# Kernel tuning notes

Hardware: AMD Instinct MI355X
Metric: run time of the kernel (lower is better)

The kernel has to match this reference:

```python
import jax, jax.numpy as jnp
import numpy as np

NEG_SLOPE = 0.01  # torch nn.LeakyReLU default


def setup_inputs() -> dict:
    key = jax.random.key(0)
    k1, k2, k3 = jax.random.split(key, 3)
    B, H, D, L = 4, 8, 64, 2048
    q = jax.random.normal(k1, (B, H, D, L), dtype=jnp.float32)
    k = jax.random.normal(k2, (B, H, D, L), dtype=jnp.float32)
    v = jax.random.normal(k3, (B, H, D, L), dtype=jnp.float32)
    return {"q": q, "k": k, "v": v}


def reference(q, k, v):
    # q, k, v: [B, H, D, L] (note: feature dim BEFORE length, as in the torch module)
    d_tensor = q.shape[2]
    scale = 1.0 / np.sqrt(d_tensor).astype(np.float32)
    # scores = LeakyReLU(q^T k / sqrt(d)) : [B, H, Lq, Lk]
    scores = jnp.einsum('bhdq,bhdk->bhqk', q, k) * scale
    scores = jax.nn.leaky_relu(scores, negative_slope=NEG_SLOPE)
    psi = jax.nn.softmax(scores, axis=-1)
    # out = (psi @ v^T)^T : [B, H, D, Lq]
    out = jnp.einsum('bhqk,bhdk->bhdq', psi, v)
    return out
```

## Files before the change

kernel.cpp:

```cpp
#include <hip/hip_runtime.h>
#include <math.h>

#define DD 64
#define LL 2048
#define TQ 128
#define TK 64
#define NTHREADS 512
#define QSCALE 0.18033688011112042f

typedef __bf16 bf16_t;
typedef __bf16 bf16x8 __attribute__((ext_vector_type(8)));
typedef float f32x16 __attribute__((ext_vector_type(16)));

struct __align__(16) SMemA {
  bf16_t Qs[TQ][72];
  bf16_t Ks[TK][72];
  bf16_t Vs[DD][72];
};
union __align__(16) SMemU {
  SMemA a;
  float Oe[TQ][65];
};

__global__ __launch_bounds__(NTHREADS, 4)
void attn_flash_bf16(const float* __restrict__ q, const float* __restrict__ k,
                     const float* __restrict__ v, float* __restrict__ out) {
  __shared__ SMemU sm;
  __shared__ float rs1[TQ];
  const int tid  = threadIdx.x;
  const int w    = tid >> 6;
  const int lane = tid & 63;
  const int l31  = lane & 31;
  const int hh   = lane >> 5;
  const int strip = w & 3;
  const int half  = w >> 2;
  const int wbase = strip * 32;
  const int lkh   = half * 32;
  const int head = blockIdx.y;
  const int q0   = blockIdx.x * TQ;
  const size_t hoff = (size_t)head * DD * LL;
  const float* qp = q + hoff;
  const float* kp = k + hoff;
  const float* vp = v + hoff;

  {
    int lq  = tid & 127;
    int d0q = (tid >> 7) * 16;
    const float* src = qp + q0 + lq;
    for (int g = 0; g < 2; ++g) {
      bf16x8 pk;
      for (int j = 0; j < 8; ++j)
        pk[j] = (bf16_t)(src[(size_t)(d0q + g * 8 + j) * LL] * QSCALE);
      *(bf16x8*)&sm.a.Qs[lq][d0q + g * 8] = pk;
    }
  }

  const int klk = tid & 63;
  const int kd0 = (tid >> 6) * 8;
  const int vd  = tid >> 3;
  const int vc8 = (tid & 7) * 8;

  float  kreg[8];
  float4 vreg[2];
  {
    const float* ks = kp + klk;
    for (int j = 0; j < 8; ++j) kreg[j] = ks[(size_t)(kd0 + j) * LL];
    vreg[0] = *(const float4*)(vp + (size_t)vd * LL + vc8);
    vreg[1] = *(const float4*)(vp + (size_t)vd * LL + vc8 + 4);
  }

  __syncthreads();
  bf16x8 bq[4];
  for (int kk = 0; kk < 4; ++kk)
    bq[kk] = *(const bf16x8*)&sm.a.Qs[wbase + l31][kk * 16 + 8 * hh];

  f32x16 oacc[2];
  for (int dt = 0; dt < 2; ++dt)
    for (int r = 0; r < 16; ++r) oacc[dt][r] = 0.f;
  float rsum = 0.f;

  for (int t = 0; t < LL / TK; ++t) {
    __syncthreads();
    {
      bf16x8 pk;
      for (int j = 0; j < 8; ++j) pk[j] = (bf16_t)kreg[j];
      *(bf16x8*)&sm.a.Ks[klk][kd0] = pk;
      bf16x8 pv;
      pv[0] = (bf16_t)vreg[0].x; pv[1] = (bf16_t)vreg[0].y;
      pv[2] = (bf16_t)vreg[0].z; pv[3] = (bf16_t)vreg[0].w;
      pv[4] = (bf16_t)vreg[1].x; pv[5] = (bf16_t)vreg[1].y;
      pv[6] = (bf16_t)vreg[1].z; pv[7] = (bf16_t)vreg[1].w;
      *(bf16x8*)&sm.a.Vs[vd][vc8] = pv;
    }
    __syncthreads();

    if (t + 1 < LL / TK) {
      const int lk0n = (t + 1) * TK;
      const float* ks = kp + lk0n + klk;
      for (int j = 0; j < 8; ++j) kreg[j] = ks[(size_t)(kd0 + j) * LL];
      vreg[0] = *(const float4*)(vp + (size_t)vd * LL + lk0n + vc8);
      vreg[1] = *(const float4*)(vp + (size_t)vd * LL + lk0n + vc8 + 4);
    }

    f32x16 st;
    for (int r = 0; r < 16; ++r) st[r] = 0.f;
    for (int kk = 0; kk < 4; ++kk) {
      bf16x8 ak = *(const bf16x8*)&sm.a.Ks[lkh + l31][kk * 16 + 8 * hh];
      st = __builtin_amdgcn_mfma_f32_32x32x16_bf16(ak, bq[kk], st, 0, 0, 0);
    }

    unsigned pb[8];
    for (int r = 0; r < 16; ++r) {
      float s = st[r];
      s = fmaxf(s, 0.01f * s);
      float p = __builtin_amdgcn_exp2f(s);
      rsum += p;
      st[r] = p;
    }
    for (int qq = 0; qq < 8; ++qq) {
      union { bf16_t b[2]; unsigned u; } pk;
      pk.b[0] = (bf16_t)st[2 * qq];
      pk.b[1] = (bf16_t)st[2 * qq + 1];
      pb[qq] = pk.u;
    }

    for (int kk2 = 0; kk2 < 2; ++kk2) {
      unsigned l0 = pb[4 * kk2 + 0], l1 = pb[4 * kk2 + 1];
      unsigned l2 = pb[4 * kk2 + 2], l3 = pb[4 * kk2 + 3];
      unsigned s0 = hh ? l0 : l2;
      unsigned s1 = hh ? l1 : l3;
      unsigned f0 = (unsigned)__shfl_xor((int)s0, 32);
      unsigned f1 = (unsigned)__shfl_xor((int)s1, 32);
      union { unsigned u[4]; bf16x8 v; } ap;
      ap.u[0] = hh ? f0 : l0;
      ap.u[1] = hh ? f1 : l1;
      ap.u[2] = hh ? l2 : f0;
      ap.u[3] = hh ? l3 : f1;
      const int lkb = lkh + kk2 * 16 + 8 * hh;
      for (int dt = 0; dt < 2; ++dt) {
        bf16x8 bv = *(const bf16x8*)&sm.a.Vs[dt * 32 + l31][lkb];
        oacc[dt] = __builtin_amdgcn_mfma_f32_32x32x16_bf16(ap.v, bv, oacc[dt], 0, 0, 0);
      }
    }
  }

  float rtot = rsum + __shfl_xor(rsum, 32);
  __syncthreads();
  if (half == 1) {
    rs1[wbase + l31] = rtot;
    for (int r = 0; r < 16; ++r) {
      int row = (r & 3) + 8 * (r >> 2) + 4 * hh;
      for (int dt = 0; dt < 2; ++dt)
        sm.Oe[wbase + row][dt * 32 + l31] = oacc[dt][r];
    }
  }
  __syncthreads();
  if (half == 0) {
    float tot = rtot + rs1[wbase + l31];
    rs1[wbase + l31] = 1.0f / tot;
    float inv[16];
    for (int r = 0; r < 16; ++r) {
      int row = (r & 3) + 8 * (r >> 2) + 4 * hh;
      inv[r] = rs1[wbase + row];
    }
    for (int r = 0; r < 16; ++r) {
      int row = (r & 3) + 8 * (r >> 2) + 4 * hh;
      for (int dt = 0; dt < 2; ++dt) {
        int col = dt * 32 + l31;
        sm.Oe[wbase + row][col] = (oacc[dt][r] + sm.Oe[wbase + row][col]) * inv[r];
      }
    }
  }
  __syncthreads();
  float* op = out + hoff + q0;
  for (int i = 0; i < 16; ++i) {
    int idx = tid + NTHREADS * i;
    int d   = idx >> 7;
    int lq  = idx & 127;
    op[(size_t)d * LL + lq] = sm.Oe[lq][d];
  }
}

extern "C" void kernel_launch(void* const* d_in, const int* in_sizes, int n_in,
                              void* d_out, int out_size, void* d_ws, size_t ws_size,
                              hipStream_t stream) {
  const float* q = (const float*)d_in[0];
  const float* k = (const float*)d_in[1];
  const float* v = (const float*)d_in[2];
  float* out = (float*)d_out;
  dim3 grid(LL / TQ, 32);
  attn_flash_bf16<<<grid, NTHREADS, 0, stream>>>(q, k, v, out);
}
```

Baseline: 144.7 us.

## Pre-convert Q/K/V to transposed bf16 and double-buffer K/V tiles

Adds a prep kernel that converts Q and K to bf16 with a length-major transposed layout and V to bf16, writing them into workspace. The attention kernel then loads 16-byte contiguous bf16 vectors instead of strided fp32 scalars, uses double-buffered K/V shared tiles so one barrier per iteration is removed, and raises wave priority around MFMA blocks. This costs an extra kernel launch and a full read/write pass over the inputs. It also depends on workspace being available, otherwise the old kernel runs.

```diff
diff --git a/kernel.cpp b/kernel.cpp
--- a/kernel.cpp
+++ b/kernel.cpp
@@ -3,6 +3,7 @@
 
 #define DD 64
 #define LL 2048
+#define HEADS 32
 #define TQ 128
 #define TK 64
 #define NTHREADS 512
@@ -11,6 +12,202 @@
 typedef __bf16 bf16_t;
 typedef __bf16 bf16x8 __attribute__((ext_vector_type(8)));
 typedef float f32x16 __attribute__((ext_vector_type(16)));
+
+__global__ __launch_bounds__(256)
+void prep_bf16(const float* __restrict__ q, const float* __restrict__ k,
+               const float* __restrict__ v, bf16_t* __restrict__ qt,
+               bf16_t* __restrict__ kt, bf16_t* __restrict__ vb) {
+  __shared__ float ld[64][65];
+  const int t = threadIdx.x;
+  const int which = blockIdx.z;
+  const int head = blockIdx.y;
+  const int l0 = blockIdx.x * 64;
+  const size_t hoff = (size_t)head * DD * LL;
+  if (which == 2) {
+    const float* src = v + hoff;
+    bf16_t* dst = vb + hoff;
+    const int lp = (t & 31) * 2;
+    const int db = (t >> 5) * 8;
+    for (int i = 0; i < 8; ++i) {
+      int d = db + i;
+      float2 x = *(const float2*)(src + (size_t)d * LL + l0 + lp);
+      union { bf16_t b[2]; unsigned u; } pk;
+      pk.b[0] = (bf16_t)x.x;
+      pk.b[1] = (bf16_t)x.y;
+      *(unsigned*)(dst + (size_t)d * LL + l0 + lp) = pk.u;
+    }
+  } else {
+    const float* src = (which == 0) ? (q + hoff) : (k + hoff);
+    bf16_t* dst = (which == 0) ? (qt + hoff) : (kt + hoff);
+    const float scale = (which == 0) ? QSCALE : 1.0f;
+    const int l = t & 63;
+    const int db = (t >> 6) * 16;
+    for (int i = 0; i < 16; ++i) {
+      int d = db + i;
+      ld[l][d] = src[(size_t)d * LL + l0 + l] * scale;
+    }
+    __syncthreads();
+    const int dp = (t & 31) * 2;
+    const int lb = (t >> 5) * 8;
+    for (int i = 0; i < 8; ++i) {
+      int lw = lb + i;
+      union { bf16_t b[2]; unsigned u; } pk;
+      pk.b[0] = (bf16_t)ld[lw][dp];
+      pk.b[1] = (bf16_t)ld[lw][dp + 1];
+      *(unsigned*)(dst + (size_t)(l0 + lw) * DD + dp) = pk.u;
+    }
+  }
+}
+
+struct __align__(16) SMemA2 {
+  bf16_t Qs[TQ][72];
+  bf16_t Ks[2][TK][72];
+  bf16_t Vs[2][DD][72];
+};
+union __align__(16) SMemU2 {
+  SMemA2 a;
+  float Oe[TQ][65];
+};
+
+__global__ __launch_bounds__(NTHREADS, 4)
+void attn_flash_bf16_v2(const bf16_t* __restrict__ qt, const bf16_t* __restrict__ kt,
+                        const bf16_t* __restrict__ vb, float* __restrict__ out) {
+  __shared__ SMemU2 sm;
+  __shared__ float rs1[TQ];
+  const int tid  = threadIdx.x;
+  const int w    = tid >> 6;
+  const int lane = tid & 63;
+  const int l31  = lane & 31;
+  const int hh   = lane >> 5;
+  const int strip = w & 3;
+  const int half  = w >> 2;
+  const int wbase = strip * 32;
+  const int lkh   = half * 32;
+  const int head = blockIdx.y;
+  const int q0   = blockIdx.x * TQ;
+  const size_t hoff = (size_t)head * DD * LL;
+  const bf16_t* qp = qt + hoff;
+  const bf16_t* kp = kt + hoff;
+  const bf16_t* vp = vb + hoff;
+
+  for (int g = 0; g < 2; ++g) {
+    int c  = tid + NTHREADS * g;
+    int lq = c >> 3;
+    int d0 = (c & 7) * 8;
+    bf16x8 x = *(const bf16x8*)(qp + (size_t)(q0 + lq) * DD + d0);
+    *(bf16x8*)&sm.a.Qs[lq][d0] = x;
+  }
+
+  const int srow = tid >> 3;
+  const int scol = (tid & 7) * 8;
+
+  bf16x8 kreg = *(const bf16x8*)(kp + (size_t)srow * DD + scol);
+  bf16x8 vreg = *(const bf16x8*)(vp + (size_t)srow * LL + scol);
+
+  __syncthreads();
+  bf16x8 bq[4];
+  for (int kk = 0; kk < 4; ++kk)
+    bq[kk] = *(const bf16x8*)&sm.a.Qs[wbase + l31][kk * 16 + 8 * hh];
+
+  f32x16 oacc[2];
+  for (int dt = 0; dt < 2; ++dt)
+    for (int r = 0; r < 16; ++r) oacc[dt][r] = 0.f;
+  float rsum = 0.f;
+
+  for (int t = 0; t < LL / TK; ++t) {
+    const int cur = t & 1;
+    *(bf16x8*)&sm.a.Ks[cur][srow][scol] = kreg;
+    *(bf16x8*)&sm.a.Vs[cur][srow][scol] = vreg;
+    __syncthreads();
+
+    if (t + 1 < LL / TK) {
+      const int lk0n = (t + 1) * TK;
+      kreg = *(const bf16x8*)(kp + (size_t)(lk0n + srow) * DD + scol);
+      vreg = *(const bf16x8*)(vp + (size_t)srow * LL + lk0n + scol);
+    }
+
+    f32x16 st;
+    for (int r = 0; r < 16; ++r) st[r] = 0.f;
+    __builtin_amdgcn_s_setprio(1);
+    for (int kk = 0; kk < 4; ++kk) {
+      bf16x8 ak = *(const bf16x8*)&sm.a.Ks[cur][lkh + l31][kk * 16 + 8 * hh];
+      st = __builtin_amdgcn_mfma_f32_32x32x16_bf16(ak, bq[kk], st, 0, 0, 0);
+    }
+    __builtin_amdgcn_s_setprio(0);
+
+    unsigned pb[8];
+    for (int r = 0; r < 16; ++r) {
+      float s = st[r];
+      s = fmaxf(s, 0.01f * s);
+      float p = __builtin_amdgcn_exp2f(s);
+      rsum += p;
+      st[r] = p;
+    }
+    for (int qq = 0; qq < 8; ++qq) {
+      union { bf16_t b[2]; unsigned u; } pk;
+      pk.b[0] = (bf16_t)st[2 * qq];
+      pk.b[1] = (bf16_t)st[2 * qq + 1];
+      pb[qq] = pk.u;
+    }
+
+    for (int kk2 = 0; kk2 < 2; ++kk2) {
+      unsigned l0 = pb[4 * kk2 + 0], l1 = pb[4 * kk2 + 1];
+      unsigned l2 = pb[4 * kk2 + 2], l3 = pb[4 * kk2 + 3];
+      unsigned s0 = hh ? l0 : l2;
+      unsigned s1 = hh ? l1 : l3;
+      unsigned f0 = (unsigned)__shfl_xor((int)s0, 32);
+      unsigned f1 = (unsigned)__shfl_xor((int)s1, 32);
+      union { unsigned u[4]; bf16x8 v; } ap;
+      ap.u[0] = hh ? f0 : l0;
+      ap.u[1] = hh ? f1 : l1;
+      ap.u[2] = hh ? l2 : f0;
+      ap.u[3] = hh ? l3 : f1;
+      const int lkb = lkh + kk2 * 16 + 8 * hh;
+      __builtin_amdgcn_s_setprio(1);
+      for (int dt = 0; dt < 2; ++dt) {
+        bf16x8 bv = *(const bf16x8*)&sm.a.Vs[cur][dt * 32 + l31][lkb];
+        oacc[dt] = __builtin_amdgcn_mfma_f32_32x32x16_bf16(ap.v, bv, oacc[dt], 0, 0, 0);
+      }
+      __builtin_amdgcn_s_setprio(0);
+    }
+  }
+
+  float rtot = rsum + __shfl_xor(rsum, 32);
+  __syncthreads();
+  if (half == 1) {
+    rs1[wbase + l31] = rtot;
+    for (int r = 0; r < 16; ++r) {
+      int row = (r & 3) + 8 * (r >> 2) + 4 * hh;
+      for (int dt = 0; dt < 2; ++dt)
+        sm.Oe[wbase + row][dt * 32 + l31] = oacc[dt][r];
+    }
+  }
+  __syncthreads();
+  if (half == 0) {
+    float tot = rtot + rs1[wbase + l31];
+    rs1[wbase + l31] = 1.0f / tot;
+    float inv[16];
+    for (int r = 0; r < 16; ++r) {
+      int row = (r & 3) + 8 * (r >> 2) + 4 * hh;
+      inv[r] = rs1[wbase + row];
+    }
+    for (int r = 0; r < 16; ++r) {
+      int row = (r & 3) + 8 * (r >> 2) + 4 * hh;
+      for (int dt = 0; dt < 2; ++dt) {
+        int col = dt * 32 + l31;
+        sm.Oe[wbase + row][col] = (oacc[dt][r] + sm.Oe[wbase + row][col]) * inv[r];
+      }
+    }
+  }
+  __syncthreads();
+  float* op = out + hoff + q0;
+  for (int i = 0; i < 16; ++i) {
+    int idx = tid + NTHREADS * i;
+    int d   = idx >> 7;
+    int lq  = idx & 127;
+    op[(size_t)d * LL + lq] = sm.Oe[lq][d];
+  }
+}
 
 struct __align__(16) SMemA {
   bf16_t Qs[TQ][72];
@@ -188,6 +385,15 @@
   const float* k = (const float*)d_in[1];
   const float* v = (const float*)d_in[2];
   float* out = (float*)d_out;
-  dim3 grid(LL / TQ, 32);
-  attn_flash_bf16<<<grid, NTHREADS, 0, stream>>>(q, k, v, out);
+  const size_t per_buf = (size_t)HEADS * DD * LL;
+  const size_t need = 3 * per_buf * sizeof(bf16_t);
+  if (d_ws && ws_size >= need) {
+    bf16_t* qt = (bf16_t*)d_ws;
+    bf16_t* kt = qt + per_buf;
+    bf16_t* vb = kt + per_buf;
+    prep_bf16<<<dim3(LL / 64, HEADS, 3), 256, 0, stream>>>(q, k, v, qt, kt, vb);
+    attn_flash_bf16_v2<<<dim3(LL / TQ, HEADS), NTHREADS, 0, stream>>>(qt, kt, vb, out);
+  } else {
+    attn_flash_bf16<<<dim3(LL / TQ, HEADS), NTHREADS, 0, stream>>>(q, k, v, out);
+  }
 }
```

Result: no change. 144.9 us (+0.2%).
